# Kernel optimization log

Hardware: AMD Instinct MI355X
Metric: run time of the kernel (lower is better)

## Reference

```python
import jax, jax.numpy as jnp
import numpy as np

SCALE = 20.0
TEMP = 1.0
POW = 0.5
SINK_TAU = 0.3
SINK_ITERS = 30
LAMBDA_LC = 1.0
EPS = 1e-12


def _l2norm(f):
    # F.normalize(f, p=2, dim=channel) * 20 ; f: [B,N,C], normalize over C
    n = jnp.sqrt(jnp.sum(f * f, axis=-1, keepdims=True))
    return f / jnp.maximum(n, EPS) * SCALE


def _sinkhorn(log_alpha, n_iters):
    # log-space Sinkhorn normalization (gumbel_sinkhorn with n_samples=1, no noise)
    def body(la, _):
        la = la - jax.nn.logsumexp(la, axis=2, keepdims=True)  # row normalize
        la = la - jax.nn.logsumexp(la, axis=1, keepdims=True)  # col normalize
        return la, None
    la, _ = jax.lax.scan(body, log_alpha, None, length=n_iters)
    return jnp.exp(la)


def setup_inputs() -> dict:
    key = jax.random.key(0)
    k1, k2 = jax.random.split(key)
    feats = jax.random.normal(k1, (16, 1024, 128), dtype=jnp.float32)
    pc0 = jax.random.normal(k2, (8, 1024, 3), dtype=jnp.float32)
    return {"feats": feats, "pc0": pc0, "epoch": 0}


def reference(feats, pc0, epoch):
    B, N, _ = pc0.shape
    f1 = _l2norm(feats[0::2])                 # [B,N,C]
    f2 = _l2norm(feats[1::2])                 # [B,N,C]
    fa = jnp.roll(f1, -1, axis=0)             # anchor feats1[(b+1)%B]

    corr_1a = jnp.einsum('bnc,bmc->bnm', f1, fa) / TEMP
    smcorr_1a = jax.nn.softmax(corr_1a, axis=2)
    f1_via_fa = jnp.einsum('bnm,bmc->bnc', smcorr_1a, fa)
    corr_1a2 = jnp.einsum('bnc,bmc->bnm', f1_via_fa, f2) / TEMP
    smcorr_1a2 = jax.nn.softmax(corr_1a2, axis=2)

    # Sinkhorn branch is under torch.no_grad()
    sink = jax.lax.stop_gradient(_sinkhorn(corr_1a2 / SINK_TAU, SINK_ITERS))

    # pairwise distance weights (no_grad)
    diff = pc0[:, :, None, :] - pc0[:, None, :, :]            # [B,N,N,3]
    dist = jax.lax.stop_gradient(jnp.sqrt(jnp.sum(diff * diff, axis=-1)) ** POW)

    corr_12 = jnp.einsum('bnc,bmc->bnm', f1, f2)
    smcorr_12 = jax.nn.softmax(corr_12 / TEMP, axis=2)

    L = dist * (smcorr_1a2 + smcorr_12)                       # L = dist*sm1a2 + dist*sm12
    loss = jnp.sum(L) / N                                     # sum over b of L.sum()/N

    eye = jnp.eye(N, dtype=sink.dtype)
    perm_to_I = 3.0 * jnp.sum(jnp.abs(eye[None] - sink)) / N
    Lc = 3.0 * jnp.sum(jnp.abs(sink - smcorr_1a2)) / N

    correct_match = jnp.sum(
        (jnp.argmax(smcorr_1a2, axis=2) == jnp.arange(N)[None, :]).astype(jnp.float32)
    )

    total_loss = loss + LAMBDA_LC * Lc
    Bf = jnp.float32(B)
    return (total_loss / Bf, loss / Bf, Lc / Bf, correct_match / Bf, perm_to_I / Bf)
```

## Files before the change

kernel.cpp:

```cpp
#include <hip/hip_runtime.h>
#include <math.h>

#define NB 8
#define NN 1024
#define NC 128
#define INV_TAU (1.0f/0.3f)
#define LOG2E 1.44269504088896340736f

typedef unsigned short u16;
typedef short bf16x8 __attribute__((ext_vector_type(8)));
typedef float f32x4 __attribute__((ext_vector_type(4)));

__device__ __forceinline__ float wsum(float v){
  #pragma unroll
  for (int o = 32; o > 0; o >>= 1) v += __shfl_xor(v, o, 64);
  return v;
}
__device__ __forceinline__ float wmax(float v){
  #pragma unroll
  for (int o = 32; o > 0; o >>= 1) v = fmaxf(v, __shfl_xor(v, o, 64));
  return v;
}
__device__ __forceinline__ float fexp2(float x){ return __builtin_amdgcn_exp2f(x); }
__device__ __forceinline__ float flog2(float x){ return __builtin_amdgcn_logf(x); }
__device__ __forceinline__ u16 f2bf(float f){
  unsigned u = __float_as_uint(f);
  return (u16)((u + 0x7FFFu + ((u >> 16) & 1u)) >> 16);
}
__device__ __forceinline__ float bf2f(u16 h){ return __uint_as_float((unsigned)h << 16); }

__device__ __forceinline__ void load16(const float* __restrict__ base, int lane, float* o){
  float4 a = *(const float4*)(base + 8 * lane);
  float4 b = *(const float4*)(base + 8 * lane + 4);
  float4 c = *(const float4*)(base + 512 + 8 * lane);
  float4 d = *(const float4*)(base + 512 + 8 * lane + 4);
  o[0]=a.x; o[1]=a.y; o[2]=a.z; o[3]=a.w; o[4]=b.x; o[5]=b.y; o[6]=b.z; o[7]=b.w;
  o[8]=c.x; o[9]=c.y; o[10]=c.z; o[11]=c.w; o[12]=d.x; o[13]=d.y; o[14]=d.z; o[15]=d.w;
}

__global__ void k_init(float* accs, float* P, float* V){
  int i = blockIdx.x * 256 + threadIdx.x;
  if (i < 160) accs[i] = 0.0f;
  P[i] = 0.0f; V[i] = 0.0f;
}

__global__ void k_normalize(const float* __restrict__ feats, float* __restrict__ f1,
                            u16* __restrict__ f1h, u16* __restrict__ f1l,
                            u16* __restrict__ f2h, u16* __restrict__ f2l){
  int vid = blockIdx.x;
  int lane = threadIdx.x;
  const float* src = feats + (size_t)vid * NC;
  float2 x = *(const float2*)(src + lane * 2);
  float s = wsum(x.x * x.x + x.y * x.y);
  float sc = 20.0f / fmaxf(sqrtf(s), 1e-12f);
  int batch = vid >> 10, n = vid & 1023;
  size_t off = ((size_t)(batch >> 1) * NN + n) * NC + 2 * lane;
  float2 y; y.x = x.x * sc; y.y = x.y * sc;
  u16 h0 = f2bf(y.x), h1 = f2bf(y.y);
  u16 l0 = f2bf(y.x - bf2f(h0)), l1 = f2bf(y.y - bf2f(h1));
  unsigned hw = (unsigned)h0 | ((unsigned)h1 << 16);
  unsigned lw = (unsigned)l0 | ((unsigned)l1 << 16);
  if (batch & 1){
    *(unsigned*)(f2h + off) = hw; *(unsigned*)(f2l + off) = lw;
  } else {
    *(float2*)(f1 + off) = y;
    *(unsigned*)(f1h + off) = hw; *(unsigned*)(f1l + off) = lw;
  }
}

__global__ __launch_bounds__(256) void k_gemm_mfma(const u16* __restrict__ Ah_g,
                                                   const u16* __restrict__ Al_g,
                                                   const u16* __restrict__ Bh_g,
                                                   const u16* __restrict__ Bl_g,
                                                   void* __restrict__ Cm,
                                                   int rollB, int q16){
  __shared__ __align__(16) u16 As_h[128][64];
  __shared__ __align__(16) u16 As_l[128][64];
  __shared__ __align__(16) u16 Bs_h[128][64];
  __shared__ __align__(16) u16 Bs_l[128][64];
  const float QS12 = 32766.0f / 400.0f;
  int b = blockIdx.z;
  int m0 = blockIdx.x * 128, n0 = blockIdx.y * 128;
  int tid = threadIdx.x, w = tid >> 6, lane = tid & 63;
  int quad = lane >> 4, l15 = lane & 15;
  int wn = (w >> 1) * 64, wm = (w & 1) * 64;
  size_t abase = (size_t)b * NN * NC;
  size_t bbase = (size_t)((b + rollB) & 7) * NN * NC;
  f32x4 z = {0.0f, 0.0f, 0.0f, 0.0f};
  f32x4 acc[4][4] = {{z,z,z,z},{z,z,z,z},{z,z,z,z},{z,z,z,z}};
  for (int kk = 0; kk < NC; kk += 64){
    #pragma unroll
    for (int i2 = 0; i2 < 4; i2++){
      int uidx = tid + 256 * i2;
      int r = uidx >> 3, u = uidx & 7;
      int su = ((u ^ (r & 7)) << 3);
      size_t goA = abase + (size_t)(n0 + r) * NC + kk + u * 8;
      size_t goB = bbase + (size_t)(m0 + r) * NC + kk + u * 8;
      *(uint4*)&As_h[r][su] = *(const uint4*)(Ah_g + goA);
      *(uint4*)&As_l[r][su] = *(const uint4*)(Al_g + goA);
      *(uint4*)&Bs_h[r][su] = *(const uint4*)(Bh_g + goB);
      *(uint4*)&Bs_l[r][su] = *(const uint4*)(Bl_g + goB);
    }
    __syncthreads();
    #pragma unroll
    for (int c = 0; c < 2; c++){
      bf16x8 ah[4], al[4], bh[4], bl[4];
      #pragma unroll
      for (int i = 0; i < 4; i++){
        int rn = wn + i * 16 + l15;
        int sn = (((c * 4 + quad) ^ (rn & 7)) << 3);
        ah[i] = *(const bf16x8*)&As_h[rn][sn];
        al[i] = *(const bf16x8*)&As_l[rn][sn];
        int rm = wm + i * 16 + l15;
        int sm = (((c * 4 + quad) ^ (rm & 7)) << 3);
        bh[i] = *(const bf16x8*)&Bs_h[rm][sm];
        bl[i] = *(const bf16x8*)&Bs_l[rm][sm];
      }
      #pragma unroll
      for (int i = 0; i < 4; i++)
        #pragma unroll
        for (int j = 0; j < 4; j++){
          acc[i][j] = __builtin_amdgcn_mfma_f32_16x16x32_bf16(ah[i], bh[j], acc[i][j], 0, 0, 0);
          acc[i][j] = __builtin_amdgcn_mfma_f32_16x16x32_bf16(ah[i], bl[j], acc[i][j], 0, 0, 0);
          acc[i][j] = __builtin_amdgcn_mfma_f32_16x16x32_bf16(al[i], bh[j], acc[i][j], 0, 0, 0);
        }
    }
    __syncthreads();
  }
  if (q16){
    short* Cb = (short*)Cm + (size_t)b * NN * NN;
    #pragma unroll
    for (int i = 0; i < 4; i++)
      #pragma unroll
      for (int j = 0; j < 4; j++)
        #pragma unroll
        for (int r = 0; r < 4; r++){
          int n = n0 + wn + i * 16 + quad * 4 + r;
          int m = m0 + wm + j * 16 + l15;
          float q = rintf(fminf(fmaxf(acc[i][j][r] * QS12, -32766.0f), 32766.0f));
          Cb[(size_t)n * NN + m] = (short)(int)q;
        }
  } else {
    float* Cb = (float*)Cm + (size_t)b * NN * NN;
    #pragma unroll
    for (int i = 0; i < 4; i++)
      #pragma unroll
      for (int j = 0; j < 4; j++)
        #pragma unroll
        for (int r = 0; r < 4; r++){
          int n = n0 + wn + i * 16 + quad * 4 + r;
          int m = m0 + wm + j * 16 + l15;
          Cb[(size_t)n * NN + m] = acc[i][j][r];
        }
  }
}

__global__ void k_rowstats(const float* __restrict__ Mb, float* __restrict__ lse){
  int row = blockIdx.x * 4 + (threadIdx.x >> 6);
  int lane = threadIdx.x & 63;
  const float* p = Mb + (size_t)row * NN;
  float x[16]; float mx = -3.402823466e38f;
  #pragma unroll
  for (int k = 0; k < 16; k++){ x[k] = p[lane + 64 * k]; mx = fmaxf(mx, x[k]); }
  mx = wmax(mx);
  float s = 0.0f;
  #pragma unroll
  for (int k = 0; k < 16; k++) s += expf(x[k] - mx);
  s = wsum(s);
  if (lane == 0) lse[row] = mx + logf(s);
}

__global__ void k_rowstats_argmax(const float* __restrict__ Mb, float* __restrict__ lse,
                                  float* __restrict__ accs){
  __shared__ float axs[4];
  int row = blockIdx.x * 4 + (threadIdx.x >> 6);
  int wid = threadIdx.x >> 6;
  int lane = threadIdx.x & 63;
  const float* p = Mb + (size_t)row * NN;
  float x[16]; float mx = -3.402823466e38f; float ax = 0.0f;
  float bm = -3.402823466e38f; int bi = 0;
  #pragma unroll
  for (int k = 0; k < 16; k++){
    x[k] = p[lane + 64 * k];
    mx = fmaxf(mx, x[k]);
    ax = fmaxf(ax, fabsf(x[k]));
    if (x[k] > bm){ bm = x[k]; bi = lane + 64 * k; }
  }
  mx = wmax(mx); ax = wmax(ax);
  #pragma unroll
  for (int o = 32; o > 0; o >>= 1){
    float om = __shfl_xor(bm, o, 64); int oi = __shfl_xor(bi, o, 64);
    if (om > bm || (om == bm && oi < bi)){ bm = om; bi = oi; }
  }
  float s = 0.0f;
  #pragma unroll
  for (int k = 0; k < 16; k++) s += expf(x[k] - mx);
  s = wsum(s);
  if (lane == 0){
    lse[row] = mx + logf(s);
    axs[wid] = ax;
    if (bi == (row & 1023)) atomicAdd(&accs[48 + (blockIdx.x & 15)], 1.0f);
  }
  __syncthreads();
  if (threadIdx.x == 0){
    float a = fmaxf(fmaxf(axs[0], axs[1]), fmaxf(axs[2], axs[3]));
    atomicMax((int*)&accs[64 + (blockIdx.x & 15)], __float_as_int(a));
  }
}

__global__ void k_scale(float* accs){
  if (threadIdx.x == 0){
    float g = 0.0f;
    for (int j = 0; j < 16; j++) g = fmaxf(g, accs[64 + j]);
    accs[80] = (g * INV_TAU * LOG2E) / 32766.0f;
  }
}

__global__ __launch_bounds__(256) void k_fva(const float* __restrict__ Mb,
                                             const float* __restrict__ lse1,
                                             const float* __restrict__ f1,
                                             float* __restrict__ fva){
  __shared__ float Ps[32][36];
  __shared__ float Bs[32][128];
  int b = blockIdx.y;
  int z = blockIdx.z;
  int n0 = blockIdx.x * 32;
  int mbase = z * 256;
  const float* Mrow = Mb + (size_t)(b * NN + n0) * NN + mbase;
  const float* fa = f1 + (size_t)((b + 1) & 7) * NN * NC + (size_t)mbase * NC;
  const float* lseb = lse1 + b * NN + n0;
  float* fvaH = fva + (size_t)z * 1048576;
  int tid = threadIdx.x;
  int ty = tid >> 5, tx = tid & 31;
  float acc[4][4] = {};
  for (int mm = 0; mm < 256; mm += 32){
    {
      int r = tid >> 3, m4 = tid & 7;
      float l = lseb[r];
      float4 v = *(const float4*)(Mrow + (size_t)r * NN + mm + m4 * 4);
      Ps[m4*4+0][r] = expf(v.x - l); Ps[m4*4+1][r] = expf(v.y - l);
      Ps[m4*4+2][r] = expf(v.z - l); Ps[m4*4+3][r] = expf(v.w - l);
    }
    #pragma unroll
    for (int i = 0; i < 4; i++){
      int t = tid + 256 * i;
      int m = t >> 5, c4 = t & 31;
      *(float4*)&Bs[m][c4 * 4] = *(const float4*)(fa + (size_t)(mm + m) * NC + c4 * 4);
    }
    __syncthreads();
    #pragma unroll 8
    for (int m = 0; m < 32; m++){
      float4 a4 = *(const float4*)&Ps[m][ty * 4];
      float4 b4 = *(const float4*)&Bs[m][tx * 4];
      acc[0][0] += a4.x*b4.x; acc[0][1] += a4.x*b4.y; acc[0][2] += a4.x*b4.z; acc[0][3] += a4.x*b4.w;
      acc[1][0] += a4.y*b4.x; acc[1][1] += a4.y*b4.y; acc[1][2] += a4.y*b4.z; acc[1][3] += a4.y*b4.w;
      acc[2][0] += a4.z*b4.x; acc[2][1] += a4.z*b4.y; acc[2][2] += a4.z*b4.z; acc[2][3] += a4.z*b4.w;
      acc[3][0] += a4.w*b4.x; acc[3][1] += a4.w*b4.y; acc[3][2] += a4.w*b4.z; acc[3][3] += a4.w*b4.w;
    }
    __syncthreads();
  }
  #pragma unroll
  for (int i = 0; i < 4; i++){
    float4 o = make_float4(acc[i][0], acc[i][1], acc[i][2], acc[i][3]);
    *(float4*)(fvaH + ((size_t)(b * NN + n0 + ty * 4 + i)) * NC + tx * 4) = o;
  }
}

__global__ __launch_bounds__(256) void k_split(const float* __restrict__ A,
                                               u16* __restrict__ H, u16* __restrict__ L){
  int g = blockIdx.x * 256 + threadIdx.x;
  float4 a = ((const float4*)A)[g];
  float4 b = ((const float4*)(A + 1048576))[g];
  float4 c = ((const float4*)(A + 2097152))[g];
  float4 d = ((const float4*)(A + 3145728))[g];
  float s[4] = { a.x + b.x + c.x + d.x, a.y + b.y + c.y + d.y,
                 a.z + b.z + c.z + d.z, a.w + b.w + c.w + d.w };
  u16 h[4], l[4];
  #pragma unroll
  for (int k = 0; k < 4; k++){
    h[k] = f2bf(s[k]);
    l[k] = f2bf(s[k] - bf2f(h[k]));
  }
  uint2 hw, lw;
  hw.x = (unsigned)h[0] | ((unsigned)h[1] << 16); hw.y = (unsigned)h[2] | ((unsigned)h[3] << 16);
  lw.x = (unsigned)l[0] | ((unsigned)l[1] << 16); lw.y = (unsigned)l[2] | ((unsigned)l[3] << 16);
  ((uint2*)H)[g] = hw; ((uint2*)L)[g] = lw;
}

__global__ __launch_bounds__(256) void k_quant_t(const float* __restrict__ Mb,
                                                 const float* __restrict__ accs,
                                                 short* __restrict__ Q,
                                                 short* __restrict__ Qt){
  __shared__ float T[64][68];
  float KQ = (INV_TAU * LOG2E) / accs[80];
  int b = blockIdx.z; int n0 = blockIdx.y * 64, m0 = blockIdx.x * 64;
  const float* src = Mb + (size_t)b * NN * NN;
  int tid = threadIdx.x;
  #pragma unroll
  for (int i = 0; i < 4; i++){
    int t = tid + 256 * i; int r = t >> 4, c4 = t & 15;
    float4 v = *(const float4*)(src + (size_t)(n0 + r) * NN + m0 + c4 * 4);
    float q0 = rintf(v.x * KQ);
    float q1 = rintf(v.y * KQ);
    float q2 = rintf(v.z * KQ);
    float q3 = rintf(v.w * KQ);
    T[r][c4*4+0] = q0; T[r][c4*4+1] = q1; T[r][c4*4+2] = q2; T[r][c4*4+3] = q3;
    int2 w;
    w.x = ((int)q0 & 0xFFFF) | ((int)q1 << 16);
    w.y = ((int)q2 & 0xFFFF) | ((int)q3 << 16);
    *(int2*)(Q + ((size_t)(b * NN + n0 + r) * NN + m0 + c4 * 4)) = w;
  }
  __syncthreads();
  #pragma unroll
  for (int i = 0; i < 4; i++){
    int t = tid + 256 * i; int r = t >> 4, c4 = t & 15;
    float q0 = T[c4*4+0][r], q1 = T[c4*4+1][r], q2 = T[c4*4+2][r], q3 = T[c4*4+3][r];
    int2 w;
    w.x = ((int)q0 & 0xFFFF) | ((int)q1 << 16);
    w.y = ((int)q2 & 0xFFFF) | ((int)q3 << 16);
    *(int2*)(Qt + ((size_t)(b * NN + m0 + r) * NN + n0 + c4 * 4)) = w;
  }
}

__global__ __launch_bounds__(256) void k_pass(const short* __restrict__ Q,
                                              const float* __restrict__ invec,
                                              float* __restrict__ outvec,
                                              const float* __restrict__ accs){
  const float IQ2 = accs[80];
  int tid = threadIdx.x, wid = tid >> 6, lane = tid & 63;
  int row = blockIdx.x * 4 + wid;
  int b = row >> 10;
  float hh[16];
  load16(invec + b * NN, lane, hh);
  const int4* qp = (const int4*)(Q + (size_t)row * NN);
  int4 wa = qp[lane], wb = qp[64 + lane];
  int qq[8] = { wa.x, wa.y, wa.z, wa.w, wb.x, wb.y, wb.z, wb.w };
  float x[16]; float mx = -3.402823466e38f;
  #pragma unroll
  for (int k = 0; k < 8; k++){
    x[2*k]   = fmaf((float)(short)(qq[k]), IQ2, hh[2*k]);
    x[2*k+1] = fmaf((float)(qq[k] >> 16),  IQ2, hh[2*k+1]);
    mx = fmaxf(mx, fmaxf(x[2*k], x[2*k+1]));
  }
  mx = wmax(mx);
  float s = 0.0f;
  #pragma unroll
  for (int k = 0; k < 16; k++) s += fexp2(x[k] - mx);
  s = wsum(s);
  if (lane == 0) outvec[row] = -(mx + flog2(s));
}

__global__ __launch_bounds__(1024) void k_final(const short* __restrict__ Q,
                                                const short* __restrict__ Q12,
                                                const float* __restrict__ lse2,
                                                const float* __restrict__ P2,
                                                const float* __restrict__ V2,
                                                const float* __restrict__ pc0,
                                                float* __restrict__ accs){
  __shared__ float pcx[1152], pcy[1152], pcz[1152];
  __shared__ float partial[3][16];
  const float IQ2 = accs[80];
  const float IQ12_2 = (400.0f / 32766.0f) * LOG2E;
  int tid = threadIdx.x, wid = tid >> 6, lane = tid & 63;
  int row = blockIdx.x * 16 + wid;
  int b = row >> 10, n = row & 1023;
  {
    int m = tid;
    const float* pg = pc0 + (size_t)b * 3072 + 3 * m;
    float px = pg[0], py = pg[1], pz = pg[2];
    int idx = m + (m >> 3);
    pcx[idx] = px; pcy[idx] = py; pcz[idx] = pz;
  }
  __syncthreads();
  const int4* qp  = (const int4*)(Q   + (size_t)row * NN);
  const int4* qp2 = (const int4*)(Q12 + (size_t)row * NN);
  int4 a1 = qp[lane],  b1 = qp[64 + lane];
  int4 a2 = qp2[lane], b2 = qp2[64 + lane];
  int q1[8] = { a1.x, a1.y, a1.z, a1.w, b1.x, b1.y, b1.z, b1.w };
  int q2[8] = { a2.x, a2.y, a2.z, a2.w, b2.x, b2.y, b2.z, b2.w };
  float L[16], c[16];
  float cmx = -3.402823466e38f;
  #pragma unroll
  for (int k = 0; k < 8; k++){
    L[2*k]   = (float)(short)(q1[k]) * IQ2;
    L[2*k+1] = (float)(q1[k] >> 16)  * IQ2;
    c[2*k]   = (float)(short)(q2[k]) * IQ12_2;
    c[2*k+1] = (float)(q2[k] >> 16)  * IQ12_2;
    cmx = fmaxf(cmx, fmaxf(c[2*k], c[2*k+1]));
  }
  cmx = wmax(cmx);
  float cs = 0.0f;
  #pragma unroll
  for (int k = 0; k < 16; k++) cs += fexp2(c[k] - cmx);
  cs = wsum(cs);
  float lse12r = cmx + flog2(cs);
  float vv[16];
  load16(V2 + b * NN, lane, vv);
  int nidx = n + (n >> 3);
  float qx = pcx[nidx], qy = pcy[nidx], qz = pcz[nidx];
  float c1row = -lse2[row] * LOG2E;
  float Prow = P2[row];
  float sl = 0.0f, slc = 0.0f, spi = 0.0f;
  #pragma unroll
  for (int k = 0; k < 16; k++){
    int m = (k < 8) ? (8 * lane + k) : (512 + 8 * lane + k - 8);
    int midx = m + (m >> 3);
    float e1 = fexp2(fmaf(L[k], 0.3f, c1row));
    float sk = fexp2(L[k] + Prow + vv[k]);
    float e2 = fexp2(c[k] - lse12r);
    float dx = qx - pcx[midx], dy = qy - pcy[midx], dz = qz - pcz[midx];
    float d = sqrtf(sqrtf(dx*dx + dy*dy + dz*dz));
    sl  += d * (e1 + e2);
    slc += fabsf(sk - e1);
    spi += fabsf(((m == n) ? 1.0f : 0.0f) - sk);
  }
  sl = wsum(sl); slc = wsum(slc); spi = wsum(spi);
  if (lane == 0){ partial[0][wid] = sl; partial[1][wid] = slc; partial[2][wid] = spi; }
  __syncthreads();
  if (tid < 3){
    float t = 0.0f;
    #pragma unroll
    for (int i = 0; i < 16; i++) t += partial[tid][i];
    atomicAdd(&accs[tid * 16 + (blockIdx.x & 15)], t);
  }
}

__global__ void k_finalize(const float* __restrict__ accs, float* __restrict__ out){
  if (threadIdx.x == 0){
    float sl = 0, slc = 0, spi = 0, scm = 0;
    for (int j = 0; j < 16; j++){
      sl += accs[j]; slc += accs[16 + j]; spi += accs[32 + j]; scm += accs[48 + j];
    }
    float loss = sl / 1024.0f;
    float Lc   = 3.0f * slc / 1024.0f;
    float perm = 3.0f * spi / 1024.0f;
    float total = loss + Lc;
    out[0] = total / 8.0f;
    out[1] = loss / 8.0f;
    out[2] = Lc / 8.0f;
    out[3] = scm / 8.0f;
    out[4] = perm / 8.0f;
  }
}

extern "C" void kernel_launch(void* const* d_in, const int* in_sizes, int n_in,
                              void* d_out, int out_size, void* d_ws, size_t ws_size,
                              hipStream_t stream){
  const float* feats = (const float*)d_in[0];
  const float* pc0   = (const float*)d_in[1];
  float* out = (float*)d_out;

  float* ws   = (float*)d_ws;
  float* f1   = ws;
  u16* f1h    = (u16*)(f1 + 1048576);
  u16* f1l    = f1h + 1048576;
  u16* f2h    = f1l + 1048576;
  u16* f2l    = f2h + 1048576;
  u16* fvh    = f2l + 1048576;
  u16* fvl    = fvh + 1048576;
  float* fva  = (float*)(fvl + 1048576);
  float* M    = fva + 4194304;
  short* Q    = (short*)(M + 8388608);
  short* Qt   = Q + 8388608;
  float* lse1 = (float*)(Qt + 8388608);
  float* lse2 = lse1 + 8192;
  float* P    = lse2 + 8192;
  float* V    = P + 8192;
  float* accs = V + 8192;
  if (ws_size < (size_t)((char*)(accs + 160) - (char*)ws)) return;

  k_init<<<32, 256, 0, stream>>>(accs, P, V);
  k_normalize<<<16384, 64, 0, stream>>>(feats, f1, f1h, f1l, f2h, f2l);
  k_gemm_mfma<<<dim3(8,8,8), 256, 0, stream>>>(f1h, f1l, f1h, f1l, M, 1, 0);
  k_rowstats<<<2048, 256, 0, stream>>>(M, lse1);
  k_fva<<<dim3(32,8,4), 256, 0, stream>>>(M, lse1, f1, fva);
  k_split<<<1024, 256, 0, stream>>>(fva, fvh, fvl);
  k_gemm_mfma<<<dim3(8,8,8), 256, 0, stream>>>(fvh, fvl, f2h, f2l, M, 0, 0);
  k_rowstats_argmax<<<2048, 256, 0, stream>>>(M, lse2, accs);
  k_scale<<<1, 64, 0, stream>>>(accs);
  k_quant_t<<<dim3(16,16,8), 256, 0, stream>>>(M, accs, Q, Qt);
  for (int it = 0; it < 30; it++){
    k_pass<<<2048, 256, 0, stream>>>(Q,  V, P, accs);
    k_pass<<<2048, 256, 0, stream>>>(Qt, P, V, accs);
  }
  k_gemm_mfma<<<dim3(8,8,8), 256, 0, stream>>>(f1h, f1l, f2h, f2l, Qt, 0, 1);
  k_final<<<512, 1024, 0, stream>>>(Q, Qt, lse2, P, V, pc0, accs);
  k_finalize<<<1, 64, 0, stream>>>(accs, out);
}
```

Baseline: 474.7 us.

## Move softmax-weighted feature GEMM onto bf16 split MFMA and enlarge Sinkhorn blocks

Replaces the scalar FP32 k_fva GEMM with an MFMA kernel that exponentiates M rows into hi/lo bf16 splits in LDS and multiplies against a pre-transposed anchor feature matrix, using three MFMA products to approximate FP32 accuracy. A new transpose kernel produces the transposed hi/lo feature copies. It also changes the Sinkhorn pass kernel to 1024-thread blocks covering 16 rows each. The split-bf16 approach trades some precision and extra workspace plus a transpose launch for much higher matrix throughput.

```diff
diff --git a/kernel.cpp b/kernel.cpp
--- a/kernel.cpp
+++ b/kernel.cpp
@@ -68,6 +68,36 @@
   }
 }
 
+__global__ __launch_bounds__(256) void k_transp(const u16* __restrict__ H,
+                                                const u16* __restrict__ L,
+                                                u16* __restrict__ TH, u16* __restrict__ TL){
+  __shared__ u16 T[64][72];
+  int b = blockIdx.z, n0 = blockIdx.y * 64, c0 = blockIdx.x * 64;
+  int tid = threadIdx.x;
+  #pragma unroll
+  for (int pass = 0; pass < 2; pass++){
+    const u16* src = (pass ? L : H) + (size_t)b * NN * NC;
+    u16* dst = (pass ? TL : TH) + (size_t)b * NC * NN;
+    #pragma unroll
+    for (int i = 0; i < 2; i++){
+      int unit = tid + 256 * i;
+      int r = unit >> 3, u = unit & 7;
+      *(uint4*)&T[r][u * 8] = *(const uint4*)(src + (size_t)(n0 + r) * NC + c0 + u * 8);
+    }
+    __syncthreads();
+    #pragma unroll
+    for (int i = 0; i < 2; i++){
+      int unit = tid + 256 * i;
+      int c = unit >> 3, nu = unit & 7;
+      u16 vals[8];
+      #pragma unroll
+      for (int k = 0; k < 8; k++) vals[k] = T[nu * 8 + k][c];
+      *(uint4*)(dst + (size_t)(c0 + c) * NN + n0 + nu * 8) = *(uint4*)vals;
+    }
+    __syncthreads();
+  }
+}
+
 __global__ __launch_bounds__(256) void k_gemm_mfma(const u16* __restrict__ Ah_g,
                                                    const u16* __restrict__ Al_g,
                                                    const u16* __restrict__ Bh_g,
@@ -216,54 +246,90 @@
   }
 }
 
-__global__ __launch_bounds__(256) void k_fva(const float* __restrict__ Mb,
-                                             const float* __restrict__ lse1,
-                                             const float* __restrict__ f1,
-                                             float* __restrict__ fva){
-  __shared__ float Ps[32][36];
-  __shared__ float Bs[32][128];
-  int b = blockIdx.y;
-  int z = blockIdx.z;
-  int n0 = blockIdx.x * 32;
-  int mbase = z * 256;
-  const float* Mrow = Mb + (size_t)(b * NN + n0) * NN + mbase;
-  const float* fa = f1 + (size_t)((b + 1) & 7) * NN * NC + (size_t)mbase * NC;
+__global__ __launch_bounds__(256) void k_fva_mfma(const float* __restrict__ Mg,
+                                                  const float* __restrict__ lse1,
+                                                  const u16* __restrict__ f1Th,
+                                                  const u16* __restrict__ f1Tl,
+                                                  float* __restrict__ fva){
+  __shared__ __align__(16) u16 Ph[128][64];
+  __shared__ __align__(16) u16 Pl[128][64];
+  __shared__ __align__(16) u16 Fh[128][64];
+  __shared__ __align__(16) u16 Fl[128][64];
+  int b = blockIdx.z, zq = blockIdx.x, ny = blockIdx.y;
+  int n0 = ny * 128, mbase = zq * 256;
+  const float* Mb = Mg + ((size_t)(b * NN + n0)) * NN + mbase;
+  const u16* fTh = f1Th + (size_t)((b + 1) & 7) * NC * NN;
+  const u16* fTl = f1Tl + (size_t)((b + 1) & 7) * NC * NN;
   const float* lseb = lse1 + b * NN + n0;
-  float* fvaH = fva + (size_t)z * 1048576;
-  int tid = threadIdx.x;
-  int ty = tid >> 5, tx = tid & 31;
-  float acc[4][4] = {};
-  for (int mm = 0; mm < 256; mm += 32){
-    {
-      int r = tid >> 3, m4 = tid & 7;
+  float* out = fva + (size_t)zq * 1048576 + ((size_t)(b * NN + n0)) * NC;
+  int tid = threadIdx.x, w = tid >> 6, lane = tid & 63;
+  int quad = lane >> 4, l15 = lane & 15;
+  int wn = (w >> 1) * 64, wc = (w & 1) * 64;
+  f32x4 z = {0.0f, 0.0f, 0.0f, 0.0f};
+  f32x4 acc[4][4] = {{z,z,z,z},{z,z,z,z},{z,z,z,z},{z,z,z,z}};
+  for (int mm = 0; mm < 256; mm += 64){
+    #pragma unroll
+    for (int i2 = 0; i2 < 4; i2++){
+      int unit = tid + 256 * i2;
+      int r = unit >> 3, u = unit & 7;
+      int su = ((u ^ (r & 7)) << 3);
       float l = lseb[r];
-      float4 v = *(const float4*)(Mrow + (size_t)r * NN + mm + m4 * 4);
-      Ps[m4*4+0][r] = expf(v.x - l); Ps[m4*4+1][r] = expf(v.y - l);
-      Ps[m4*4+2][r] = expf(v.z - l); Ps[m4*4+3][r] = expf(v.w - l);
-    }
-    #pragma unroll
-    for (int i = 0; i < 4; i++){
-      int t = tid + 256 * i;
-      int m = t >> 5, c4 = t & 31;
-      *(float4*)&Bs[m][c4 * 4] = *(const float4*)(fa + (size_t)(mm + m) * NC + c4 * 4);
+      const float* mp = Mb + (size_t)r * NN + mm + u * 8;
+      float4 v0 = *(const float4*)mp, v1 = *(const float4*)(mp + 4);
+      float p[8] = { fexp2((v0.x - l) * LOG2E), fexp2((v0.y - l) * LOG2E),
+                     fexp2((v0.z - l) * LOG2E), fexp2((v0.w - l) * LOG2E),
+                     fexp2((v1.x - l) * LOG2E), fexp2((v1.y - l) * LOG2E),
+                     fexp2((v1.z - l) * LOG2E), fexp2((v1.w - l) * LOG2E) };
+      u16 h[8], lo[8];
+      #pragma unroll
+      for (int k = 0; k < 8; k++){ h[k] = f2bf(p[k]); lo[k] = f2bf(p[k] - bf2f(h[k])); }
+      uint4 hw, lw;
+      hw.x = (unsigned)h[0] | ((unsigned)h[1] << 16);  hw.y = (unsigned)h[2] | ((unsigned)h[3] << 16);
+      hw.z = (unsigned)h[4] | ((unsigned)h[5] << 16);  hw.w = (unsigned)h[6] | ((unsigned)h[7] << 16);
+      lw.x = (unsigned)lo[0] | ((unsigned)lo[1] << 16); lw.y = (unsigned)lo[2] | ((unsigned)lo[3] << 16);
+      lw.z = (unsigned)lo[4] | ((unsigned)lo[5] << 16); lw.w = (unsigned)lo[6] | ((unsigned)lo[7] << 16);
+      *(uint4*)&Ph[r][su] = hw;
+      *(uint4*)&Pl[r][su] = lw;
+      size_t fo = (size_t)r * NN + mbase + mm + u * 8;
+      *(uint4*)&Fh[r][su] = *(const uint4*)(fTh + fo);
+      *(uint4*)&Fl[r][su] = *(const uint4*)(fTl + fo);
     }
     __syncthreads();
-    #pragma unroll 8
-    for (int m = 0; m < 32; m++){
-      float4 a4 = *(const float4*)&Ps[m][ty * 4];
-      float4 b4 = *(const float4*)&Bs[m][tx * 4];
-      acc[0][0] += a4.x*b4.x; acc[0][1] += a4.x*b4.y; acc[0][2] += a4.x*b4.z; acc[0][3] += a4.x*b4.w;
-      acc[1][0] += a4.y*b4.x; acc[1][1] += a4.y*b4.y; acc[1][2] += a4.y*b4.z; acc[1][3] += a4.y*b4.w;
-      acc[2][0] += a4.z*b4.x; acc[2][1] += a4.z*b4.y; acc[2][2] += a4.z*b4.z; acc[2][3] += a4.z*b4.w;
-      acc[3][0] += a4.w*b4.x; acc[3][1] += a4.w*b4.y; acc[3][2] += a4.w*b4.z; acc[3][3] += a4.w*b4.w;
+    #pragma unroll
+    for (int c2 = 0; c2 < 2; c2++){
+      bf16x8 ph[4], pl[4], fh[4], fl[4];
+      #pragma unroll
+      for (int i = 0; i < 4; i++){
+        int rn = wn + i * 16 + l15;
+        int sn = (((c2 * 4 + quad) ^ (rn & 7)) << 3);
+        ph[i] = *(const bf16x8*)&Ph[rn][sn];
+        pl[i] = *(const bf16x8*)&Pl[rn][sn];
+        int rc = wc + i * 16 + l15;
+        int sc = (((c2 * 4 + quad) ^ (rc & 7)) << 3);
+        fh[i] = *(const bf16x8*)&Fh[rc][sc];
+        fl[i] = *(const bf16x8*)&Fl[rc][sc];
+      }
+      #pragma unroll
+      for (int i = 0; i < 4; i++)
+        #pragma unroll
+        for (int j = 0; j < 4; j++){
+          acc[i][j] = __builtin_amdgcn_mfma_f32_16x16x32_bf16(ph[i], fh[j], acc[i][j], 0, 0, 0);
+          acc[i][j] = __builtin_amdgcn_mfma_f32_16x16x32_bf16(ph[i], fl[j], acc[i][j], 0, 0, 0);
+          acc[i][j] = __builtin_amdgcn_mfma_f32_16x16x32_bf16(pl[i], fh[j], acc[i][j], 0, 0, 0);
+        }
     }
     __syncthreads();
   }
   #pragma unroll
-  for (int i = 0; i < 4; i++){
-    float4 o = make_float4(acc[i][0], acc[i][1], acc[i][2], acc[i][3]);
-    *(float4*)(fvaH + ((size_t)(b * NN + n0 + ty * 4 + i)) * NC + tx * 4) = o;
-  }
+  for (int i = 0; i < 4; i++)
+    #pragma unroll
+    for (int j = 0; j < 4; j++)
+      #pragma unroll
+      for (int r = 0; r < 4; r++){
+        int n = wn + i * 16 + quad * 4 + r;
+        int c = wc + j * 16 + l15;
+        out[(size_t)n * NC + c] = acc[i][j][r];
+      }
 }
 
 __global__ __launch_bounds__(256) void k_split(const float* __restrict__ A,
@@ -322,13 +388,13 @@
   }
 }
 
-__global__ __launch_bounds__(256) void k_pass(const short* __restrict__ Q,
-                                              const float* __restrict__ invec,
-                                              float* __restrict__ outvec,
-                                              const float* __restrict__ accs){
+__global__ __launch_bounds__(1024) void k_pass(const short* __restrict__ Q,
+                                               const float* __restrict__ invec,
+                                               float* __restrict__ outvec,
+                                               const float* __restrict__ accs){
   const float IQ2 = accs[80];
   int tid = threadIdx.x, wid = tid >> 6, lane = tid & 63;
-  int row = blockIdx.x * 4 + wid;
+  int row = blockIdx.x * 16 + wid;
   int b = row >> 10;
   float hh[16];
   load16(invec + b * NN, lane, hh);
@@ -456,7 +522,9 @@
   u16* f1l    = f1h + 1048576;
   u16* f2h    = f1l + 1048576;
   u16* f2l    = f2h + 1048576;
-  u16* fvh    = f2l + 1048576;
+  u16* f1Th   = f2l + 1048576;
+  u16* f1Tl   = f1Th + 1048576;
+  u16* fvh    = f1Tl + 1048576;
   u16* fvl    = fvh + 1048576;
   float* fva  = (float*)(fvl + 1048576);
   float* M    = fva + 4194304;
@@ -471,17 +539,18 @@
 
   k_init<<<32, 256, 0, stream>>>(accs, P, V);
   k_normalize<<<16384, 64, 0, stream>>>(feats, f1, f1h, f1l, f2h, f2l);
+  k_transp<<<dim3(2,16,8), 256, 0, stream>>>(f1h, f1l, f1Th, f1Tl);
   k_gemm_mfma<<<dim3(8,8,8), 256, 0, stream>>>(f1h, f1l, f1h, f1l, M, 1, 0);
   k_rowstats<<<2048, 256, 0, stream>>>(M, lse1);
-  k_fva<<<dim3(32,8,4), 256, 0, stream>>>(M, lse1, f1, fva);
+  k_fva_mfma<<<dim3(4,8,8), 256, 0, stream>>>(M, lse1, f1Th, f1Tl, fva);
   k_split<<<1024, 256, 0, stream>>>(fva, fvh, fvl);
   k_gemm_mfma<<<dim3(8,8,8), 256, 0, stream>>>(fvh, fvl, f2h, f2l, M, 0, 0);
   k_rowstats_argmax<<<2048, 256, 0, stream>>>(M, lse2, accs);
   k_scale<<<1, 64, 0, stream>>>(accs);
   k_quant_t<<<dim3(16,16,8), 256, 0, stream>>>(M, accs, Q, Qt);
   for (int it = 0; it < 30; it++){
-    k_pass<<<2048, 256, 0, stream>>>(Q,  V, P, accs);
-    k_pass<<<2048, 256, 0, stream>>>(Qt, P, V, accs);
+    k_pass<<<512, 1024, 0, stream>>>(Q,  V, P, accs);
+    k_pass<<<512, 1024, 0, stream>>>(Qt, P, V, accs);
   }
   k_gemm_mfma<<<dim3(8,8,8), 256, 0, stream>>>(f1h, f1l, f2h, f2l, Qt, 0, 1);
   k_final<<<512, 1024, 0, stream>>>(Q, Qt, lse2, P, V, pc0, accs);
```

Result: faster. 461.4 us (-2.8%).
